# Kernel optimization log

Hardware: AMD Instinct MI355X
Metric: run time of the kernel (lower is better)

Reference implementation:

```python
import jax, jax.numpy as jnp
import numpy as np

D = 1024
H = 16
HD = D // H
FF = 4 * D
LN_EPS = 1e-5


def _layernorm(x, g, b):
    mu = jnp.mean(x, axis=-1, keepdims=True)
    var = jnp.mean(jnp.square(x - mu), axis=-1, keepdims=True)
    return (x - mu) / jnp.sqrt(var + LN_EPS) * g + b


def setup_inputs() -> dict:
    key = jax.random.key(0)
    ks = jax.random.split(key, 17)
    s = 0.02
    inp = {
        "x": jax.random.normal(ks[0], (2, 2048, D), dtype=jnp.float32),
        "Wq": jax.random.normal(ks[1], (D, D), dtype=jnp.float32) * s,
        "bq": jnp.zeros((D,), jnp.float32),
        "Wk": jax.random.normal(ks[2], (D, D), dtype=jnp.float32) * s,
        "bk": jnp.zeros((D,), jnp.float32),
        "Wv": jax.random.normal(ks[3], (D, D), dtype=jnp.float32) * s,
        "bv": jnp.zeros((D,), jnp.float32),
        "Wo": jax.random.normal(ks[4], (D, D), dtype=jnp.float32) * s,
        "bo": jnp.zeros((D,), jnp.float32),
        "ln1_g": jnp.ones((D,), jnp.float32),
        "ln1_b": jnp.zeros((D,), jnp.float32),
        "W1": jax.random.normal(ks[5], (D, FF), dtype=jnp.float32) * s,
        "b1": jnp.zeros((FF,), jnp.float32),
        "W2": jax.random.normal(ks[6], (FF, D), dtype=jnp.float32) * s,
        "b2": jnp.zeros((D,), jnp.float32),
        "ln2_g": jnp.ones((D,), jnp.float32),
        "ln2_b": jnp.zeros((D,), jnp.float32),
    }
    return inp


def reference(x, Wq, bq, Wk, bk, Wv, bv, Wo, bo, ln1_g, ln1_b, W1, b1, W2, b2, ln2_g, ln2_b):
    bs, seq, _ = x.shape
    # qkv projections -> [b, h, s, hd]
    def split_heads(t):
        return t.reshape(bs, seq, H, HD).transpose(0, 2, 1, 3)
    q = split_heads(x @ Wq + bq)
    k = split_heads(x @ Wk + bk)
    v = split_heads(x @ Wv + bv)
    # causal attention (explicit, matching source math)
    scores = jnp.einsum('bhqd,bhkd->bhqk', q, k) / jnp.sqrt(jnp.float32(HD))
    causal = jnp.tril(jnp.ones((seq, seq), dtype=bool))
    scores = jnp.where(causal, scores, -jnp.inf)
    attn = jax.nn.softmax(scores, axis=-1)
    ctx = jnp.einsum('bhqk,bhkd->bhqd', attn, v)
    ctx = ctx.transpose(0, 2, 1, 3).reshape(bs, seq, D)
    attn_out = ctx @ Wo + bo
    # residual + LN1
    h = _layernorm(attn_out + x, ln1_g, ln1_b)
    # GELU MLP (exact erf gelu, torch nn.GELU default)
    ffn = jax.nn.gelu(h @ W1 + b1, approximate=False) @ W2 + b2
    # residual + LN2
    out = _layernorm(ffn + h, ln2_g, ln2_b)
    return out
```

## Files before the change

### kernel.cpp

```cpp
#include <hip/hip_runtime.h>

#define D_MODEL 1024
#define SEQ 2048
#define NHEAD 16
#define HDIM 64
#define FF_DIM 4096
#define NTOK 4096

using bf16x8 = __attribute__((ext_vector_type(8))) short;
using f32x4  = __attribute__((ext_vector_type(4))) float;
typedef unsigned short ushort_t;

__device__ __forceinline__ unsigned short f2bu(float f) {
    unsigned int u = __float_as_uint(f);
    unsigned int r = u + 0x7FFFu + ((u >> 16) & 1u);
    return (unsigned short)(r >> 16);
}
__device__ __forceinline__ float b2f(unsigned short u) {
    union { unsigned int i; float f; } x;
    x.i = ((unsigned int)u) << 16;
    return x.f;
}

typedef __attribute__((address_space(1))) const unsigned int* gas_ptr;
typedef __attribute__((address_space(3))) unsigned int* las_ptr;
__device__ __forceinline__ void gload_lds16(const void* g, void* l) {
    __builtin_amdgcn_global_load_lds((gas_ptr)g, (las_ptr)l, 16, 0, 0);
}

__device__ __forceinline__ float gelu_f(float x) {
    float z = 1.59576912f * x * (1.f + 0.044715f * x * x);
    float t = __expf(z);
    float th = (t - 1.f) / (t + 1.f);
    return 0.5f * x * (1.f + th);
}

__global__ void cast_f32_to_bf16(const float* __restrict__ in, ushort_t* __restrict__ out, int n8) {
    int i = blockIdx.x * blockDim.x + threadIdx.x;
    if (i >= n8) return;
    const float4* p = (const float4*)in + (size_t)i * 2;
    float4 a = p[0], b = p[1];
    uint4 o;
    o.x = (unsigned)f2bu(a.x) | ((unsigned)f2bu(a.y) << 16);
    o.y = (unsigned)f2bu(a.z) | ((unsigned)f2bu(a.w) << 16);
    o.z = (unsigned)f2bu(b.x) | ((unsigned)f2bu(b.y) << 16);
    o.w = (unsigned)f2bu(b.z) | ((unsigned)f2bu(b.w) << 16);
    ((uint4*)out)[i] = o;
}

__global__ void transpose_f32_to_bf16(const float* __restrict__ in, ushort_t* __restrict__ out, int R, int C) {
    __shared__ float tile[64][65];
    int bx = blockIdx.x * 64, by = blockIdx.y * 64;
    int tx = threadIdx.x & 63, ty = threadIdx.x >> 6;
#pragma unroll
    for (int i = 0; i < 64; i += 4)
        tile[ty + i][tx] = in[(size_t)(by + ty + i) * C + bx + tx];
    __syncthreads();
#pragma unroll
    for (int i = 0; i < 64; i += 4)
        out[(size_t)(bx + ty + i) * R + by + tx] = f2bu(tile[tx][ty + i]);
}

__global__ __launch_bounds__(256)
void gemm_bf16(const ushort_t* __restrict__ A, const ushort_t* __restrict__ Bt,
               const float* __restrict__ bias, int bias_per_row,
               ushort_t* __restrict__ outb, float* __restrict__ outf,
               int M, int N, int K, float out_scale, int do_gelu) {
    __shared__ char lds[2 * 128 * 128];
    char* Al = lds;
    char* Bl = lds + 128 * 128;
    const int tid = threadIdx.x;
    const int l = tid & 63, w = tid >> 6;
    const int wr = w >> 1, wc = w & 1;
    const int g = l >> 4, l15 = l & 15;
    const int m0 = blockIdx.x * 128, n0 = blockIdx.y * 128;

    f32x4 acc[4][4] = {};
    const int nk = K >> 6;
    const int srow = l >> 3;
    const int scol = (l & 7) * 8;
    const ushort_t* Ab = A + (size_t)(m0 + w * 32 + srow) * K + scol;
    const ushort_t* Bb = Bt + (size_t)(n0 + w * 32 + srow) * K + scol;

    for (int kt = 0; kt < nk; ++kt) {
        __syncthreads();
        const size_t ko = (size_t)kt * 64;
#pragma unroll
        for (int c = 0; c < 4; ++c) {
            gload_lds16(Ab + (size_t)c * 8 * K + ko, Al + (w * 4 + c) * 1024);
            gload_lds16(Bb + (size_t)c * 8 * K + ko, Bl + (w * 4 + c) * 1024);
        }
        __syncthreads();
#pragma unroll
        for (int ks = 0; ks < 2; ks++) {
            bf16x8 af[4];
#pragma unroll
            for (int m = 0; m < 4; m++)
                af[m] = *(const bf16x8*)(Al + (wr * 64 + m * 16 + l15) * 128 + (ks * 4 + g) * 16);
#pragma unroll
            for (int n = 0; n < 4; n++) {
                bf16x8 bfr = *(const bf16x8*)(Bl + (wc * 64 + n * 16 + l15) * 128 + (ks * 4 + g) * 16);
#pragma unroll
                for (int m = 0; m < 4; m++)
                    acc[m][n] = __builtin_amdgcn_mfma_f32_16x16x32_bf16(af[m], bfr, acc[m][n], 0, 0, 0);
            }
        }
    }
#pragma unroll
    for (int m = 0; m < 4; m++) {
        int row0 = m0 + wr * 64 + m * 16 + g * 4;
#pragma unroll
        for (int n = 0; n < 4; n++) {
            int col = n0 + wc * 64 + n * 16 + l15;
            float bc = bias_per_row ? 0.f : bias[col];
#pragma unroll
            for (int jj = 0; jj < 4; jj++) {
                int row = row0 + jj;
                float v = acc[m][n][jj] + (bias_per_row ? bias[row] : bc);
                v *= out_scale;
                if (do_gelu) v = gelu_f(v);
                size_t idx = (size_t)row * N + col;
                if (outb) outb[idx] = f2bu(v);
                else      outf[idx] = v;
            }
        }
    }
}

__global__ __launch_bounds__(256)
void attn_fwd(const ushort_t* __restrict__ qg, const ushort_t* __restrict__ kg,
              const ushort_t* __restrict__ vtg, ushort_t* __restrict__ ctx) {
    __shared__ char plds[4 * 16 * 144];
    const int tid = threadIdx.x;
    const int l = tid & 63, w = tid >> 6;
    const int g = l >> 4, l15 = l & 15;
    const int bid = blockIdx.x;
    const int QBi = bid & 31, h = (bid >> 5) & 15, b = bid >> 9;
    const int q0 = QBi * 64;
    const int qrow = b * SEQ + q0 + w * 16 + l15;
    const int q_local = w * 16 + l15;

    const ushort_t* qp = qg + (size_t)qrow * D_MODEL + h * HDIM + g * 8;
    bf16x8 qf0 = *(const bf16x8*)qp;
    bf16x8 qf1 = *(const bf16x8*)(qp + 32);

    f32x4 O[4] = {};
    float m_run = -1e30f, l_run = 0.f;
    char* pl = plds + w * (16 * 144) + l15 * 144;

    for (int t = 0; t <= QBi; ++t) {
        const int kv0 = t * 64;
        f32x4 s[4];
#pragma unroll
        for (int md = 0; md < 4; ++md) {
            const ushort_t* kp = kg + (size_t)(b * SEQ + kv0 + md * 16 + l15) * D_MODEL + h * HDIM + g * 8;
            f32x4 z = {0.f, 0.f, 0.f, 0.f};
            z = __builtin_amdgcn_mfma_f32_16x16x32_bf16(*(const bf16x8*)kp, qf0, z, 0, 0, 0);
            z = __builtin_amdgcn_mfma_f32_16x16x32_bf16(*(const bf16x8*)(kp + 32), qf1, z, 0, 0, 0);
            s[md] = z;
        }
        if (t == QBi) {
#pragma unroll
            for (int md = 0; md < 4; ++md)
#pragma unroll
                for (int jj = 0; jj < 4; jj++) {
                    int kvl = md * 16 + g * 4 + jj;
                    if (kvl > q_local) s[md][jj] = -1e30f;
                }
        }
        float pmax = -1e30f;
#pragma unroll
        for (int md = 0; md < 4; ++md)
#pragma unroll
            for (int jj = 0; jj < 4; jj++) pmax = fmaxf(pmax, s[md][jj]);
        pmax = fmaxf(pmax, __shfl_xor(pmax, 16));
        pmax = fmaxf(pmax, __shfl_xor(pmax, 32));
        float mnew = fmaxf(m_run, pmax);
        float sc = __expf(m_run - mnew);
        float rsum = 0.f;
#pragma unroll
        for (int md = 0; md < 4; ++md) {
            float p0 = __expf(s[md][0] - mnew);
            float p1 = __expf(s[md][1] - mnew);
            float p2 = __expf(s[md][2] - mnew);
            float p3 = __expf(s[md][3] - mnew);
            rsum += (p0 + p1) + (p2 + p3);
            uint2 pk;
            pk.x = (unsigned)f2bu(p0) | ((unsigned)f2bu(p1) << 16);
            pk.y = (unsigned)f2bu(p2) | ((unsigned)f2bu(p3) << 16);
            *(uint2*)(pl + (md * 16 + g * 4) * 2) = pk;
        }
        rsum += __shfl_xor(rsum, 16);
        rsum += __shfl_xor(rsum, 32);
        l_run = l_run * sc + rsum;
        m_run = mnew;
#pragma unroll
        for (int md = 0; md < 4; ++md) {
            O[md][0] *= sc; O[md][1] *= sc; O[md][2] *= sc; O[md][3] *= sc;
        }
#pragma unroll
        for (int ks = 0; ks < 2; ++ks) {
            bf16x8 pf = *(const bf16x8*)(pl + ks * 64 + g * 16);
#pragma unroll
            for (int md = 0; md < 4; ++md) {
                const ushort_t* vp = vtg + (size_t)(h * HDIM + md * 16 + l15) * NTOK + b * SEQ + kv0 + ks * 32 + g * 8;
                O[md] = __builtin_amdgcn_mfma_f32_16x16x32_bf16(*(const bf16x8*)vp, pf, O[md], 0, 0, 0);
            }
        }
    }
    float rl = 1.f / l_run;
#pragma unroll
    for (int md = 0; md < 4; ++md) {
        uint2 o;
        o.x = (unsigned)f2bu(O[md][0] * rl) | ((unsigned)f2bu(O[md][1] * rl) << 16);
        o.y = (unsigned)f2bu(O[md][2] * rl) | ((unsigned)f2bu(O[md][3] * rl) << 16);
        *(uint2*)(ctx + (size_t)qrow * D_MODEL + h * HDIM + md * 16 + g * 4) = o;
    }
}

__global__ __launch_bounds__(256)
void ln_kernel(const ushort_t* __restrict__ a, const ushort_t* __restrict__ resb,
               const float* __restrict__ resf,
               const float* __restrict__ gam, const float* __restrict__ bet,
               ushort_t* __restrict__ outb, float* __restrict__ outf) {
    const int w = threadIdx.x >> 6, l = threadIdx.x & 63;
    const int row = blockIdx.x * 4 + w;
    const size_t base = (size_t)row * D_MODEL + l * 16;
    float r[16];
    int4 av0 = *(const int4*)(a + base);
    int4 av1 = *(const int4*)(a + base + 8);
    const unsigned short* u0 = (const unsigned short*)&av0;
    const unsigned short* u1 = (const unsigned short*)&av1;
#pragma unroll
    for (int i = 0; i < 8; i++) { r[i] = b2f(u0[i]); r[8 + i] = b2f(u1[i]); }
    if (resf) {
        const float4* rp = (const float4*)(resf + base);
#pragma unroll
        for (int i = 0; i < 4; i++) {
            float4 f = rp[i];
            r[i * 4 + 0] += f.x; r[i * 4 + 1] += f.y; r[i * 4 + 2] += f.z; r[i * 4 + 3] += f.w;
        }
    } else {
        int4 rv0 = *(const int4*)(resb + base);
        int4 rv1 = *(const int4*)(resb + base + 8);
        const unsigned short* v0 = (const unsigned short*)&rv0;
        const unsigned short* v1 = (const unsigned short*)&rv1;
#pragma unroll
        for (int i = 0; i < 8; i++) { r[i] += b2f(v0[i]); r[8 + i] += b2f(v1[i]); }
    }
    float s = 0.f;
#pragma unroll
    for (int i = 0; i < 16; i++) s += r[i];
#pragma unroll
    for (int m = 1; m < 64; m <<= 1) s += __shfl_xor(s, m);
    float mu = s * (1.f / 1024.f);
    float v = 0.f;
#pragma unroll
    for (int i = 0; i < 16; i++) { float d = r[i] - mu; v += d * d; }
#pragma unroll
    for (int m = 1; m < 64; m <<= 1) v += __shfl_xor(v, m);
    float rstd = rsqrtf(v * (1.f / 1024.f) + 1e-5f);
    float o[16];
    const float4* gp = (const float4*)(gam + l * 16);
    const float4* bp = (const float4*)(bet + l * 16);
#pragma unroll
    for (int i = 0; i < 4; i++) {
        float4 gv = gp[i], bv = bp[i];
        o[i * 4 + 0] = (r[i * 4 + 0] - mu) * rstd * gv.x + bv.x;
        o[i * 4 + 1] = (r[i * 4 + 1] - mu) * rstd * gv.y + bv.y;
        o[i * 4 + 2] = (r[i * 4 + 2] - mu) * rstd * gv.z + bv.z;
        o[i * 4 + 3] = (r[i * 4 + 3] - mu) * rstd * gv.w + bv.w;
    }
    if (outb) {
        uint4 w0, w1;
        unsigned* pw0 = (unsigned*)&w0;
        unsigned* pw1 = (unsigned*)&w1;
#pragma unroll
        for (int i = 0; i < 4; i++) {
            pw0[i] = (unsigned)f2bu(o[i * 2]) | ((unsigned)f2bu(o[i * 2 + 1]) << 16);
            pw1[i] = (unsigned)f2bu(o[8 + i * 2]) | ((unsigned)f2bu(o[8 + i * 2 + 1]) << 16);
        }
        *(uint4*)(outb + base) = w0;
        *(uint4*)(outb + base + 8) = w1;
    } else {
        float4* op = (float4*)(outf + base);
#pragma unroll
        for (int i = 0; i < 4; i++)
            op[i] = make_float4(o[i * 4], o[i * 4 + 1], o[i * 4 + 2], o[i * 4 + 3]);
    }
}

extern "C" void kernel_launch(void* const* d_in, const int* in_sizes, int n_in,
                              void* d_out, int out_size, void* d_ws, size_t ws_size,
                              hipStream_t stream) {
    const float* x     = (const float*)d_in[0];
    const float* Wq    = (const float*)d_in[1];
    const float* bq    = (const float*)d_in[2];
    const float* Wk    = (const float*)d_in[3];
    const float* bk    = (const float*)d_in[4];
    const float* Wv    = (const float*)d_in[5];
    const float* bv    = (const float*)d_in[6];
    const float* Wo    = (const float*)d_in[7];
    const float* bo    = (const float*)d_in[8];
    const float* ln1_g = (const float*)d_in[9];
    const float* ln1_b = (const float*)d_in[10];
    const float* W1    = (const float*)d_in[11];
    const float* b1    = (const float*)d_in[12];
    const float* W2    = (const float*)d_in[13];
    const float* b2    = (const float*)d_in[14];
    const float* ln2_g = (const float*)d_in[15];
    const float* ln2_b = (const float*)d_in[16];
    float* out = (float*)d_out;

    char* ws = (char*)d_ws;
    const size_t SZ = (size_t)NTOK * D_MODEL * 2;
    ushort_t* xb  = (ushort_t*)(ws + 0 * SZ);
    ushort_t* qb  = (ushort_t*)(ws + 1 * SZ);
    ushort_t* kb  = (ushort_t*)(ws + 2 * SZ);
    ushort_t* vt  = (ushort_t*)(ws + 3 * SZ);
    ushort_t* ctx = (ushort_t*)(ws + 4 * SZ);
    ushort_t* aob = (ushort_t*)(ws + 5 * SZ);
    ushort_t* hb  = (ushort_t*)(ws + 6 * SZ);
    char* wts = ws + 7 * SZ;
    ushort_t* wqt = (ushort_t*)(wts + 0x000000);
    ushort_t* wkt = (ushort_t*)(wts + 0x200000);
    ushort_t* wvt = (ushort_t*)(wts + 0x400000);
    ushort_t* wot = (ushort_t*)(wts + 0x600000);
    ushort_t* w1t = (ushort_t*)(wts + 0x800000);
    ushort_t* w2t = (ushort_t*)(wts + 0x1000000);
    ushort_t* f1b = (ushort_t*)(ws + 0 * SZ);
    ushort_t* f2b = (ushort_t*)(ws + 4 * SZ);
    if (ws_size < (size_t)(7 * SZ) + 0x1800000) return;

    cast_f32_to_bf16<<<2048, 256, 0, stream>>>(x, xb, NTOK * D_MODEL / 8);
    transpose_f32_to_bf16<<<dim3(16, 16), 256, 0, stream>>>(Wq, wqt, 1024, 1024);
    transpose_f32_to_bf16<<<dim3(16, 16), 256, 0, stream>>>(Wk, wkt, 1024, 1024);
    transpose_f32_to_bf16<<<dim3(16, 16), 256, 0, stream>>>(Wv, wvt, 1024, 1024);
    transpose_f32_to_bf16<<<dim3(16, 16), 256, 0, stream>>>(Wo, wot, 1024, 1024);
    transpose_f32_to_bf16<<<dim3(64, 16), 256, 0, stream>>>(W1, w1t, 1024, 4096);
    transpose_f32_to_bf16<<<dim3(16, 64), 256, 0, stream>>>(W2, w2t, 4096, 1024);

    gemm_bf16<<<dim3(32, 8), 256, 0, stream>>>(xb, wqt, bq, 0, qb, nullptr, 4096, 1024, 1024, 0.125f, 0);
    gemm_bf16<<<dim3(32, 8), 256, 0, stream>>>(xb, wkt, bk, 0, kb, nullptr, 4096, 1024, 1024, 1.f, 0);
    gemm_bf16<<<dim3(8, 32), 256, 0, stream>>>(wvt, xb, bv, 1, vt, nullptr, 1024, 4096, 1024, 1.f, 0);

    attn_fwd<<<1024, 256, 0, stream>>>(qb, kb, vt, ctx);

    gemm_bf16<<<dim3(32, 8), 256, 0, stream>>>(ctx, wot, bo, 0, aob, nullptr, 4096, 1024, 1024, 1.f, 0);
    ln_kernel<<<1024, 256, 0, stream>>>(aob, nullptr, x, ln1_g, ln1_b, hb, nullptr);
    gemm_bf16<<<dim3(32, 32), 256, 0, stream>>>(hb, w1t, b1, 0, f1b, nullptr, 4096, 4096, 1024, 1.f, 1);
    gemm_bf16<<<dim3(32, 8), 256, 0, stream>>>(f1b, w2t, b2, 0, f2b, nullptr, 4096, 1024, 4096, 1.f, 0);
    ln_kernel<<<1024, 256, 0, stream>>>(f2b, hb, nullptr, ln2_g, ln2_b, nullptr, out);
}
```

Baseline: 647.6 us.

## Prefetch K/V tiles into registers and remap attention blocks across XCDs

```diff
diff --git a/kernel.cpp b/kernel.cpp
--- a/kernel.cpp
+++ b/kernel.cpp
@@ -135,7 +135,12 @@
     const int l = tid & 63, w = tid >> 6;
     const int g = l >> 4, l15 = l & 15;
     const int bid = blockIdx.x;
-    const int QBi = bid & 31, h = (bid >> 5) & 15, b = bid >> 9;
+    const int xcd = bid & 7;
+    const int slot = bid >> 3;
+    const int QBi = slot & 31;
+    const int grp = slot >> 5;
+    const int h = xcd + 8 * (grp & 1);
+    const int b = grp >> 1;
     const int q0 = QBi * 64;
     const int qrow = b * SEQ + q0 + w * 16 + l15;
     const int q_local = w * 16 + l15;
@@ -144,20 +149,46 @@
     bf16x8 qf0 = *(const bf16x8*)qp;
     bf16x8 qf1 = *(const bf16x8*)(qp + 32);
 
+    const ushort_t* kbase = kg + ((size_t)(b * SEQ + l15) * D_MODEL) + h * HDIM + g * 8;
+    const ushort_t* vbase = vtg + (size_t)(h * HDIM + l15) * NTOK + b * SEQ + g * 8;
+
     f32x4 O[4] = {};
     float m_run = -1e30f, l_run = 0.f;
     char* pl = plds + w * (16 * 144) + l15 * 144;
 
+    bf16x8 kf[8];
+    bf16x8 vf[8];
+#pragma unroll
+    for (int md = 0; md < 4; ++md) {
+        const ushort_t* kp = kbase + (size_t)(md * 16) * D_MODEL;
+        kf[2 * md]     = *(const bf16x8*)kp;
+        kf[2 * md + 1] = *(const bf16x8*)(kp + 32);
+    }
+
     for (int t = 0; t <= QBi; ++t) {
         const int kv0 = t * 64;
+#pragma unroll
+        for (int md = 0; md < 4; ++md) {
+            const ushort_t* vp = vbase + (size_t)(md * 16) * NTOK + kv0;
+            vf[2 * md]     = *(const bf16x8*)vp;
+            vf[2 * md + 1] = *(const bf16x8*)(vp + 32);
+        }
         f32x4 s[4];
 #pragma unroll
         for (int md = 0; md < 4; ++md) {
-            const ushort_t* kp = kg + (size_t)(b * SEQ + kv0 + md * 16 + l15) * D_MODEL + h * HDIM + g * 8;
             f32x4 z = {0.f, 0.f, 0.f, 0.f};
-            z = __builtin_amdgcn_mfma_f32_16x16x32_bf16(*(const bf16x8*)kp, qf0, z, 0, 0, 0);
-            z = __builtin_amdgcn_mfma_f32_16x16x32_bf16(*(const bf16x8*)(kp + 32), qf1, z, 0, 0, 0);
+            z = __builtin_amdgcn_mfma_f32_16x16x32_bf16(kf[2 * md], qf0, z, 0, 0, 0);
+            z = __builtin_amdgcn_mfma_f32_16x16x32_bf16(kf[2 * md + 1], qf1, z, 0, 0, 0);
             s[md] = z;
+        }
+        {
+            const int tn = (t < QBi) ? (t + 1) : t;
+#pragma unroll
+            for (int md = 0; md < 4; ++md) {
+                const ushort_t* kp = kbase + (size_t)(tn * 64 + md * 16) * D_MODEL;
+                kf[2 * md]     = *(const bf16x8*)kp;
+                kf[2 * md + 1] = *(const bf16x8*)(kp + 32);
+            }
         }
         if (t == QBi) {
 #pragma unroll
@@ -202,10 +233,8 @@
         for (int ks = 0; ks < 2; ++ks) {
             bf16x8 pf = *(const bf16x8*)(pl + ks * 64 + g * 16);
 #pragma unroll
-            for (int md = 0; md < 4; ++md) {
-                const ushort_t* vp = vtg + (size_t)(h * HDIM + md * 16 + l15) * NTOK + b * SEQ + kv0 + ks * 32 + g * 8;
-                O[md] = __builtin_amdgcn_mfma_f32_16x16x32_bf16(*(const bf16x8*)vp, pf, O[md], 0, 0, 0);
-            }
+            for (int md = 0; md < 4; ++md)
+                O[md] = __builtin_amdgcn_mfma_f32_16x16x32_bf16(vf[2 * md + ks], pf, O[md], 0, 0, 0);
         }
     }
     float rl = 1.f / l_run;
```

After: 593.0 us. -8.4%, faster.
